# Kernel optimization log

Measured on AMD Instinct MI355X. Metric: run time of the kernel, lower is better.

## Reference

```python
import jax, jax.numpy as jnp
from jax import lax
import numpy as np

GAMMA = 0.5
LENS = 0.3
B_J0 = 0.1
# eval-mode BN with running_mean=0, running_var=1, weight=0.1, bias=0 -> pure scale
BN_SCALE = 0.1 / np.sqrt(1.0 + 1e-5)


def _gaussian(x, mu, sigma):
    return jnp.exp(-(x - mu) ** 2 / (2.0 * sigma ** 2)) / np.sqrt(2.0 * np.pi) / sigma


@jax.custom_vjp
def act_fun_adp(x):
    return (x > 0).astype(x.dtype)


def _act_fwd(x):
    return act_fun_adp(x), x


def _act_bwd(x, g):
    scale, hight = 6.0, 0.15
    temp = (_gaussian(x, 0.0, LENS) * (1.0 + hight)
            - _gaussian(x, LENS, scale * LENS) * hight
            - _gaussian(x, -LENS, scale * LENS) * hight)
    return (g * temp * GAMMA,)


act_fun_adp.defvjp(_act_fwd, _act_bwd)


def _lin(x, w, b):
    return x @ w.T + b


def _mem_update_adp(inp, mem, spk, tau_adp, tau_m, b):
    b = tau_adp * b + (1.0 - tau_adp) * spk
    B = B_J0 + 1.8 * b
    mem = mem + (-mem + inp) * tau_m
    spk = act_fun_adp(mem - B)
    mem = (1.0 - spk) * mem
    return mem, spk, b


def _snn(inputs, h, p):
    (w1x, b1x, w1r, b1r, w1m, b1m, w1a, b1a,
     w2x, b2x, w2r, b2r, w2m, b2m, w2a, b2a,
     w3x, b3x, w3m, b3m) = p

    def step(h, x):
        mem1, spk1, bb1, mem2, spk2, bb2, mem3 = h
        dense1 = BN_SCALE * _lin(x, w1x, b1x) + BN_SCALE * _lin(spk1, w1r, b1r)
        tauM1 = jax.nn.sigmoid(_lin(jnp.concatenate([dense1, mem1], -1), w1m, b1m))
        tauA1 = jax.nn.sigmoid(_lin(jnp.concatenate([dense1, bb1], -1), w1a, b1a))
        nmem1, nspk1, nbb1 = _mem_update_adp(dense1, mem1, spk1, tauA1, tauM1, bb1)
        # dropout in eval mode = identity; layer2_r uses PREVIOUS spk1 (h[1]) as in source
        dense2 = BN_SCALE * _lin(nspk1, w2x, b2x) + BN_SCALE * _lin(spk1, w2r, b2r)
        tauM2 = jax.nn.sigmoid(_lin(jnp.concatenate([dense2, mem2], -1), w2m, b2m))
        tauA2 = jax.nn.sigmoid(_lin(jnp.concatenate([dense2, bb2], -1), w2a, b2a))
        nmem2, nspk2, nbb2 = _mem_update_adp(dense2, mem2, spk2, tauA2, tauM2, bb2)
        dense3 = BN_SCALE * _lin(nspk2, w3x, b3x)
        tauM3 = jax.nn.sigmoid(_lin(jnp.concatenate([dense3, mem3], -1), w3m, b3m))
        nmem3 = (1.0 - tauM3) * mem3 + dense3 * tauM3
        out = jax.nn.log_softmax(nmem3, axis=1)
        return (nmem1, nspk1, nbb1, nmem2, nspk2, nbb2, nmem3), out

    xs = jnp.swapaxes(inputs, 0, 1)  # [T, B, Din]
    hT, outs = lax.scan(step, h, xs)
    return outs, hT  # outs: [T, B, O]


def setup_inputs() -> dict:
    key = jax.random.key(0)
    B, T, DIN, H, O = 128, 100, 700, 1024, 20
    ks = jax.random.split(key, 16)
    d = {
        'inputs': jax.random.normal(ks[0], (B, T, DIN), jnp.float32),
        'h0': jnp.zeros((B, H)), 'h1': jnp.zeros((B, H)), 'h2': jnp.zeros((B, H)),
        'h3': jnp.zeros((B, H)), 'h4': jnp.zeros((B, H)), 'h5': jnp.zeros((B, H)),
        'h6': jnp.zeros((B, O)),
        'w1x': jax.random.normal(ks[1], (H, DIN)) * 0.03,
        'b1x': jnp.zeros((H,)),
        'w1r': jax.random.normal(ks[2], (H, H)) * 0.03,
        'b1r': jnp.zeros((H,)),
        'w1m': jax.random.normal(ks[3], (H, 2 * H)) * 0.02,
        'b1m': jnp.zeros((H,)),
        'w1a': jax.random.normal(ks[4], (H, 2 * H)) * 0.02,
        'b1a': jnp.zeros((H,)),
        'w2x': jax.random.normal(ks[5], (H, H)) * 0.03,
        'b2x': jnp.zeros((H,)),
        'w2r': jax.random.normal(ks[6], (H, H)) * 0.03,
        'b2r': jnp.zeros((H,)),
        'w2m': jax.random.normal(ks[7], (H, 2 * H)) * 0.02,
        'b2m': jnp.zeros((H,)),
        'w2a': jax.random.normal(ks[8], (H, 2 * H)) * 0.02,
        'b2a': jnp.zeros((H,)),
        'w3x': jax.random.normal(ks[9], (O, H)) * 0.03,
        'b3x': jnp.zeros((O,)),
        'w3m': jax.random.normal(ks[10], (O, 2 * O)) * 0.02,
        'b3m': jnp.zeros((O,)),
    }
    return d


def reference(inputs, h0, h1, h2, h3, h4, h5, h6,
              w1x, b1x, w1r, b1r, w1m, b1m, w1a, b1a,
              w2x, b2x, w2r, b2r, w2m, b2m, w2a, b2a,
              w3x, b3x, w3m, b3m):
    h = (h0, h1, h2, h3, h4, h5, h6)
    p = (w1x, b1x, w1r, b1r, w1m, b1m, w1a, b1a,
         w2x, b2x, w2r, b2r, w2m, b2m, w2a, b2a,
         w3x, b3x, w3m, b3m)
    outs, hT = _snn(inputs, h, p)
    return (outs,) + hT
```

## Files before the change

### kernel.cpp

```cpp
#include <hip/hip_runtime.h>
#include <cmath>


namespace {

constexpr int BB = 128, TT = 100, DIN = 700, HH = 1024, OO = 20;
constexpr int BH = BB * HH;
constexpr int XP = 704;
constexpr float SBN = 0.09999950000374996f;

typedef __attribute__((ext_vector_type(8))) __bf16 bf16x8;
typedef __attribute__((ext_vector_type(4))) float f32x4;

__device__ __forceinline__ float sigm(float x) { return 1.f / (1.f + expf(-x)); }

__device__ __forceinline__ unsigned short f2bf(float x) {
  union { float f; unsigned u; } a; a.f = x;
  unsigned u = a.u; u += 0x7fffu + ((u >> 16) & 1u);
  return (unsigned short)(u >> 16);
}
__device__ __forceinline__ float bf2f(unsigned short h) {
  union { unsigned u; float f; } a; a.u = ((unsigned)h) << 16; return a.f;
}


struct MSeg {
  const unsigned short* Ah; const unsigned short* Al;
  const unsigned short* Wh; const unsigned short* Wl;
  float* P;
  int ldk, KS, nsplit, nblkn;
};
struct MArgs { MSeg s[6]; int bstart[7]; int nseg; };

__global__ __launch_bounds__(256)
void mfma_seg(MArgs ma) {
  int bid = blockIdx.x, si = 0;
  while (si + 1 < ma.nseg && bid >= ma.bstart[si + 1]) si++;
  MSeg sg = ma.s[si]; bid -= ma.bstart[si];
  const int nb = bid / sg.nsplit, sp = bid - nb * sg.nsplit;
  const int n0 = nb * 64;
  const int kbeg = sp * sg.KS, kend = kbeg + sg.KS;
  const int lane = threadIdx.x & 63, wave = threadIdx.x >> 6;
  const int wm = (wave >> 1) * 64, wn = (wave & 1) * 32;
  const int quad = lane >> 4, r16 = lane & 15;
  const int ldk = sg.ldk;
  const int nkb = ldk >> 5;
  const bool three = (sg.Al != nullptr);
  const unsigned short* ah = sg.Ah + (size_t)(wm + r16) * ldk + quad * 8;
  const unsigned short* al = three ? sg.Al + (size_t)(wm + r16) * ldk + quad * 8 : ah;
  const size_t tb = (size_t)((n0 + wn) >> 4) * nkb * 512 + (size_t)lane * 8;
  const unsigned short* wh = sg.Wh + tb;
  const unsigned short* wl = sg.Wl + tb;

  f32x4 acc[4][2];
#pragma unroll
  for (int i = 0; i < 4; i++)
#pragma unroll
    for (int j = 0; j < 2; j++) acc[i][j] = (f32x4){0.f, 0.f, 0.f, 0.f};

  auto loadf = [&](int k, bf16x8* Ab, bf16x8* ALb, bf16x8* Bb, bf16x8* BLb) {
    const int kb = k >> 5;
#pragma unroll
    for (int mt = 0; mt < 4; mt++)
      Ab[mt] = *(const bf16x8*)(ah + (size_t)mt * 16 * ldk + k);
#pragma unroll
    for (int nt = 0; nt < 2; nt++) {
      Bb[nt] = *(const bf16x8*)(wh + ((size_t)nt * nkb + kb) * 512);
      BLb[nt] = *(const bf16x8*)(wl + ((size_t)nt * nkb + kb) * 512);
    }
    if (three) {
#pragma unroll
      for (int mt = 0; mt < 4; mt++)
        ALb[mt] = *(const bf16x8*)(al + (size_t)mt * 16 * ldk + k);
    }
  };
  auto domfma = [&](bf16x8* Ab, bf16x8* ALb, bf16x8* Bb, bf16x8* BLb) {
#pragma unroll
    for (int mt = 0; mt < 4; mt++)
#pragma unroll
      for (int nt = 0; nt < 2; nt++) {
        acc[mt][nt] = __builtin_amdgcn_mfma_f32_16x16x32_bf16(Ab[mt], Bb[nt], acc[mt][nt], 0, 0, 0);
        acc[mt][nt] = __builtin_amdgcn_mfma_f32_16x16x32_bf16(Ab[mt], BLb[nt], acc[mt][nt], 0, 0, 0);
        if (three)
          acc[mt][nt] = __builtin_amdgcn_mfma_f32_16x16x32_bf16(ALb[mt], Bb[nt], acc[mt][nt], 0, 0, 0);
      }
  };

  bf16x8 A0[4], L0[4], B0[2], C0[2];
  bf16x8 A1[4], L1[4], B1[2], C1[2];
  int k = kbeg;
  loadf(k, A0, L0, B0, C0);
  while (true) {
    int k1 = k + 32;
    bool more1 = k1 < kend;
    if (more1) loadf(k1, A1, L1, B1, C1);
    domfma(A0, L0, B0, C0);
    if (!more1) break;
    int k2 = k1 + 32;
    bool more2 = k2 < kend;
    if (more2) loadf(k2, A0, L0, B0, C0);
    domfma(A1, L1, B1, C1);
    if (!more2) break;
    k = k2;
  }

  const int outl = n0 >> 10;
  const int col0 = (n0 & 1023) + wn;
  float* P = sg.P + (size_t)(outl * sg.nsplit + sp) * BH;
#pragma unroll
  for (int mt = 0; mt < 4; mt++)
#pragma unroll
    for (int nt = 0; nt < 2; nt++)
#pragma unroll
      for (int r = 0; r < 4; r++)
        P[(size_t)(wm + mt * 16 + quad * 4 + r) * 1024 + col0 + nt * 16 + r16] = acc[mt][nt][r];
}

struct CJob { const float* src; int ldsrc, rows, cols; unsigned short* dh; unsigned short* dl; int lddst; float scale; };
struct CArgs { CJob j[16]; int bstart[17]; int njob; };

__global__ __launch_bounds__(256)
void cvt_pack(CArgs ca) {
  int bid = blockIdx.x, ji = 0;
  while (ji + 1 < ca.njob && bid >= ca.bstart[ji + 1]) ji++;
  CJob j = ca.j[ji]; bid -= ca.bstart[ji];
  size_t total = (size_t)j.rows * j.lddst;
  size_t base = ((size_t)bid * 256 + threadIdx.x) * 4;
  const int nkb = j.lddst >> 5;
#pragma unroll
  for (int e = 0; e < 4; e++) {
    size_t i = base + e;
    if (i >= total) break;
    size_t tile = i >> 9;
    int within = (int)(i & 511);
    int lane = within >> 3, jj = within & 7;
    int r16 = lane & 15, quad = lane >> 4;
    int ntile = (int)(tile / nkb), kb = (int)(tile - (size_t)ntile * nkb);
    int r = ntile * 16 + r16;
    int c = kb * 32 + quad * 8 + jj;
    float v = (c < j.cols) ? j.scale * j.src[(size_t)r * j.ldsrc + c] : 0.f;
    unsigned short hh = f2bf(v);
    j.dh[i] = hh;
    j.dl[i] = f2bf(v - bf2f(hh));
  }
}

__global__ __launch_bounds__(256)
void init_state(const float* h0, const float* h1, const float* h2, const float* h3,
                const float* h4, const float* h5, const float* h6, const float* inputs,
                float* mem1, float* spk1, float* bb1, float* mem2, float* spk2, float* bb2,
                float* mem3, unsigned short* spk1bf,
                unsigned short* m1h, unsigned short* m1l, unsigned short* b1h, unsigned short* b1l,
                unsigned short* m2h, unsigned short* m2l, unsigned short* b2h, unsigned short* b2l,
                unsigned short* xh0, unsigned short* xl0) {
  int idx = blockIdx.x * 256 + threadIdx.x;
  if (idx < BH) {
    float v;
    v = h0[idx]; mem1[idx] = v; { unsigned short h = f2bf(v); m1h[idx] = h; m1l[idx] = f2bf(v - bf2f(h)); }
    v = h1[idx]; spk1[idx] = v; spk1bf[idx] = f2bf(v);
    v = h2[idx]; bb1[idx] = v;  { unsigned short h = f2bf(v); b1h[idx] = h; b1l[idx] = f2bf(v - bf2f(h)); }
    v = h3[idx]; mem2[idx] = v; { unsigned short h = f2bf(v); m2h[idx] = h; m2l[idx] = f2bf(v - bf2f(h)); }
    spk2[idx] = h4[idx];
    v = h5[idx]; bb2[idx] = v;  { unsigned short h = f2bf(v); b2h[idx] = h; b2l[idx] = f2bf(v - bf2f(h)); }
  }
  if (idx < BB * OO) mem3[idx] = h6[idx];
  if (idx < BB * XP) {
    int b = idx / XP, c = idx - b * XP;
    float v = (c < DIN) ? inputs[(size_t)b * TT * DIN + c] : 0.f;
    unsigned short hh = f2bf(v);
    xh0[idx] = hh; xl0[idx] = f2bf(v - bf2f(hh));
  }
}

__global__ __launch_bounds__(256)
void ew1m(const float* Pbuf, const float* b1x, const float* b1r,
          const float* cb1m, const float* cb1a,
          float* mem1, float* spk1, float* bb1, unsigned short* spk1bf,
          unsigned short* m1h, unsigned short* m1l, unsigned short* b1h_, unsigned short* b1l_) {
  int idx = blockIdx.x * 256 + threadIdx.x;
  int n = idx & (HH - 1);
  constexpr int D1S[6]  = {0, 1, 6, 7, 8, 9};
  constexpr int T1MS[10] = {2, 3, 10, 11, 12, 13, 30, 31, 32, 33};
  constexpr int T1AS[10] = {4, 5, 14, 15, 16, 17, 34, 35, 36, 37};
  float d1 = SBN * (b1x[n] + b1r[n]);
#pragma unroll
  for (int i = 0; i < 6; i++) d1 += Pbuf[(size_t)D1S[i] * BH + idx];
  float pm = cb1m[n];
#pragma unroll
  for (int i = 0; i < 10; i++) pm += Pbuf[(size_t)T1MS[i] * BH + idx];
  float pa = cb1a[n];
#pragma unroll
  for (int i = 0; i < 10; i++) pa += Pbuf[(size_t)T1AS[i] * BH + idx];
  float tM = sigm(pm), tA = sigm(pa);
  float spo = spk1[idx], bo = bb1[idx], mo = mem1[idx];
  float nb = tA * bo + (1.f - tA) * spo;
  float Bth = 0.1f + 1.8f * nb;
  float nm = mo + (d1 - mo) * tM;
  float sp = (nm - Bth) > 0.f ? 1.f : 0.f;
  nm = (1.f - sp) * nm;
  mem1[idx] = nm; spk1[idx] = sp; bb1[idx] = nb;
  spk1bf[idx] = f2bf(sp);
  { unsigned short h = f2bf(nm); m1h[idx] = h; m1l[idx] = f2bf(nm - bf2f(h)); }
  { unsigned short h = f2bf(nb); b1h_[idx] = h; b1l_[idx] = f2bf(nb - bf2f(h)); }
}

__global__ __launch_bounds__(1024)
void ew2l3m(const float* Pbuf, const float* b2x, const float* b2r,
            const float* cb2m, const float* cb2a,
            float* mem2, float* spk2, float* bb2, float* mem3,
            unsigned short* m2h, unsigned short* m2l, unsigned short* b2h_, unsigned short* b2l_,
            const float* w3x, const float* b3x, const float* w3m, const float* b3m,
            float* outs, const float* inputs, unsigned short* xh_next, unsigned short* xl_next,
            int t) {
  int b = blockIdx.x;
  int n = threadIdx.x;
  size_t idx = (size_t)b * HH + n;
  constexpr int D2S[8]  = {18, 19, 20, 21, 46, 47, 48, 49};
  constexpr int T2MS[12] = {22, 23, 24, 25, 38, 39, 40, 41, 50, 51, 52, 53};
  constexpr int T2AS[12] = {26, 27, 28, 29, 42, 43, 44, 45, 54, 55, 56, 57};
  float d2 = SBN * (b2x[n] + b2r[n]);
#pragma unroll
  for (int i = 0; i < 8; i++) d2 += Pbuf[(size_t)D2S[i] * BH + idx];
  float pm = cb2m[n];
#pragma unroll
  for (int i = 0; i < 12; i++) pm += Pbuf[(size_t)T2MS[i] * BH + idx];
  float pa = cb2a[n];
#pragma unroll
  for (int i = 0; i < 12; i++) pa += Pbuf[(size_t)T2AS[i] * BH + idx];
  float tM = sigm(pm), tA = sigm(pa);
  float spo = spk2[idx], bo = bb2[idx], mo = mem2[idx];
  float nb = tA * bo + (1.f - tA) * spo;
  float Bth = 0.1f + 1.8f * nb;
  float nm = mo + (d2 - mo) * tM;
  float sp = (nm - Bth) > 0.f ? 1.f : 0.f;
  nm = (1.f - sp) * nm;
  mem2[idx] = nm; spk2[idx] = sp; bb2[idx] = nb;
  { unsigned short h = f2bf(nm); m2h[idx] = h; m2l[idx] = f2bf(nm - bf2f(h)); }
  { unsigned short h = f2bf(nb); b2h_[idx] = h; b2l_[idx] = f2bf(nb - bf2f(h)); }

  if (t + 1 < TT && n < XP) {
    float v = (n < DIN) ? inputs[((size_t)b * TT + (t + 1)) * DIN + n] : 0.f;
    unsigned short hh = f2bf(v);
    xh_next[b * XP + n] = hh;
    xl_next[b * XP + n] = f2bf(v - bf2f(hh));
  }

  __shared__ float smsp[HH];
  __shared__ float d3s[OO];
  __shared__ float nm3s[OO];
  smsp[n] = sp;
  __syncthreads();

  int wv = n >> 6, ln = n & 63;
  for (int o = wv; o < OO; o += 16) {
    float s = 0.f;
    for (int j = ln; j < HH; j += 64) s += smsp[j] * w3x[(size_t)o * HH + j];
    for (int off = 32; off > 0; off >>= 1) s += __shfl_down(s, off, 64);
    if (ln == 0) d3s[o] = SBN * (s + b3x[o]);
  }
  __syncthreads();

  if (n < OO) {
    float acc = b3m[n];
#pragma unroll
    for (int k = 0; k < OO; k++) acc += d3s[k] * w3m[n * 40 + k];
#pragma unroll
    for (int k = 0; k < OO; k++) acc += mem3[b * OO + k] * w3m[n * 40 + 20 + k];
    float tau = sigm(acc);
    nm3s[n] = (1.f - tau) * mem3[b * OO + n] + d3s[n] * tau;
  }
  __syncthreads();

  if (n < OO) {
    float mx = -1e30f;
#pragma unroll
    for (int k = 0; k < OO; k++) mx = fmaxf(mx, nm3s[k]);
    float se = 0.f;
#pragma unroll
    for (int k = 0; k < OO; k++) se += expf(nm3s[k] - mx);
    float lse = mx + logf(se);
    outs[((size_t)t * BB + b) * OO + n] = nm3s[n] - lse;
    mem3[b * OO + n] = nm3s[n];
  }
}


struct Seg {
  const float* A; const float* W; float* P;
  int lda, ldw, ldp, K, KS, nsplit, mblks, nblks, nbound, xmap, xoff;
  float scale;
};
constexpr int MAXSEG = 13;
struct SegArgs { Seg s[MAXSEG]; int bstart[MAXSEG + 1]; int nseg; };

__global__ __launch_bounds__(256)
void seg_gemm(SegArgs sa) {
  int bid = blockIdx.x;
  int si = 0;
  while (si + 1 < sa.nseg && bid >= sa.bstart[si + 1]) si++;
  const Seg sg = sa.s[si];
  bid -= sa.bstart[si];
  const int per_m = sg.nblks * sg.nsplit;
  const int mb = bid / per_m;
  const int rr = bid - mb * per_m;
  const int nb = rr / sg.nsplit;
  const int sp = rr - nb * sg.nsplit;
  const int m0 = mb * 128, n0 = nb * 32;
  const int kbeg = sp * sg.KS;
  const int kend = min(sg.K, kbeg + sg.KS);

  __shared__ float As[32][132];
  __shared__ float Ws[32][36];

  const int t = threadIdx.x;
  const int cg = t & 7;
  const int rg = t >> 3;

  float acc[4][4];
#pragma unroll
  for (int i = 0; i < 4; i++)
#pragma unroll
    for (int j = 0; j < 4; j++) acc[i][j] = 0.f;

  for (int k0 = kbeg; k0 < kend; k0 += 32) {
#pragma unroll
    for (int i = 0; i < 4; i++) {
      int fl = t + i * 256;
      int row = fl >> 3, kq = fl & 7;
      int kg = k0 + kq * 4;
      float4 v = make_float4(0.f, 0.f, 0.f, 0.f);
      if (kg < kend) {
        const float* src = sg.xmap
            ? sg.A + ((size_t)(m0 + row) * TT + sg.xoff) * DIN + kg
            : sg.A + (size_t)(m0 + row) * sg.lda + kg;
        v = *(const float4*)src;
      }
      As[kq * 4 + 0][row] = v.x;
      As[kq * 4 + 1][row] = v.y;
      As[kq * 4 + 2][row] = v.z;
      As[kq * 4 + 3][row] = v.w;
    }
    {
      int n = t >> 3, kq = t & 7;
      int kg = k0 + kq * 4;
      float4 v = make_float4(0.f, 0.f, 0.f, 0.f);
      if (kg < kend && (n0 + n) < sg.nbound)
        v = *(const float4*)(sg.W + (size_t)(n0 + n) * sg.ldw + kg);
      Ws[kq * 4 + 0][n] = v.x;
      Ws[kq * 4 + 1][n] = v.y;
      Ws[kq * 4 + 2][n] = v.z;
      Ws[kq * 4 + 3][n] = v.w;
    }
    __syncthreads();
#pragma unroll
    for (int kk = 0; kk < 32; kk++) {
      float4 av = *(const float4*)&As[kk][rg * 4];
      float4 wv = *(const float4*)&Ws[kk][cg * 4];
      acc[0][0] += av.x * wv.x; acc[0][1] += av.x * wv.y; acc[0][2] += av.x * wv.z; acc[0][3] += av.x * wv.w;
      acc[1][0] += av.y * wv.x; acc[1][1] += av.y * wv.y; acc[1][2] += av.y * wv.z; acc[1][3] += av.y * wv.w;
      acc[2][0] += av.z * wv.x; acc[2][1] += av.z * wv.y; acc[2][2] += av.z * wv.z; acc[2][3] += av.z * wv.w;
      acc[3][0] += av.w * wv.x; acc[3][1] += av.w * wv.y; acc[3][2] += av.w * wv.z; acc[3][3] += av.w * wv.w;
    }
    __syncthreads();
  }
  float* P = sg.P + ((size_t)sp * sg.mblks * 128 + m0) * sg.ldp;
#pragma unroll
  for (int i = 0; i < 4; i++) {
    float4 v = make_float4(sg.scale * acc[i][0], sg.scale * acc[i][1],
                           sg.scale * acc[i][2], sg.scale * acc[i][3]);
    *(float4*)&P[(size_t)(rg * 4 + i) * sg.ldp + n0 + cg * 4] = v;
  }
}

struct TJob { const float* src; float* dst; int rows, cols, ntc; };
struct TArgs { TJob j[4]; int tstart[5]; };

__global__ __launch_bounds__(256)
void transpose4(TArgs ta) {
  int bid = blockIdx.x;
  int ji = 0;
  while (ji + 1 < 4 && bid >= ta.tstart[ji + 1]) ji++;
// ... 463 lines not shown
    ta.j[0] = TJob{w1r, w1rT, HH, HH, 32};
    ta.j[1] = TJob{w2r, w2rT, HH, HH, 32};
    ta.j[2] = TJob{w2x, w2xT, HH, HH, 32};
    ta.j[3] = TJob{w1x, w1xT, HH, DIN, 22};
    ta.tstart[0] = 0; ta.tstart[1] = 1024; ta.tstart[2] = 2048;
    ta.tstart[3] = 3072; ta.tstart[4] = 3072 + 32 * 22;
    transpose4<<<ta.tstart[4], 256, 0, stream>>>(ta);
  }
  bias_prep<<<1024, 256, 0, stream>>>(b1x, b1r, b2x, b2r, w1m, b1m, w1a, b1a,
                                      w2m, b2m, w2a, b2a, cb1m, cb1a, cb2m, cb2a);
  {
    SegArgs sa{};
    int nb = 0, c = 0;
    auto add = [&](const float* A, int lda, const float* W, int ldw, int nbound,
                   float* P, int ldp, int nblks) {
      sa.s[c] = Seg{A, W, P, lda, ldw, ldp, HH, HH, 1, 8, nblks, nbound, 0, 0, 1.0f};
      sa.bstart[c] = nb; nb += 8 * nblks; c++;
    };
    add(w1m, 2048, w1rT, 1024, 1024, G1mT, 1024, 32);
    add(w1a, 2048, w1rT, 1024, 1024, G1aT, 1024, 32);
    add(w1m, 2048, w1xT, 1024, DIN, H1MT, 704, 22);
    add(w1a, 2048, w1xT, 1024, DIN, H1AT, 704, 22);
    add(w2m, 2048, w2rT, 1024, 1024, G2rmT, 1024, 32);
    add(w2a, 2048, w2rT, 1024, 1024, G2raT, 1024, 32);
    add(w2m, 2048, w2xT, 1024, 1024, G2xmT, 1024, 32);
    add(w2a, 2048, w2xT, 1024, 1024, G2xaT, 1024, 32);
    sa.bstart[c] = nb; sa.nseg = c;
    seg_gemm<<<nb, 256, 0, stream>>>(sa);
  }

  for (int t = 0; t < TT; ++t) {
    {
      SegArgs sa{};
      int nb = 0, c = 0;
      auto add = [&](const float* A, int lda, int xmap, const float* W, int ldw,
                     int K, int KS, int slot, float scale) {
        sa.s[c] = Seg{A, W, Pbuf + (size_t)slot * BH, lda, ldw, 1024, K, KS, 2, 1, 32,
                      1024, xmap, t, scale};
        sa.bstart[c] = nb; nb += 64; c++;
      };
      add(inputs, 0, 1, w1x, DIN, DIN, 352, 0, SBN);
      add(spk1, 1024, 0, w1r, 1024, 1024, 512, 2, SBN);
      add(inputs, 0, 1, H1MT, 704, DIN, 352, 4, SBN);
      add(spk1, 1024, 0, G1mT, 1024, 1024, 512, 6, SBN);
      add(mem1, 1024, 0, w1m + 1024, 2048, 1024, 512, 8, 1.0f);
      add(inputs, 0, 1, H1AT, 704, DIN, 352, 10, SBN);
      add(spk1, 1024, 0, G1aT, 1024, 1024, 512, 12, SBN);
      add(bb1, 1024, 0, w1a + 1024, 2048, 1024, 512, 14, 1.0f);
      add(spk1, 1024, 0, w2r, 1024, 1024, 512, 16, SBN);
      add(spk1, 1024, 0, G2rmT, 1024, 1024, 512, 18, SBN);
      add(mem2, 1024, 0, w2m + 1024, 2048, 1024, 512, 20, 1.0f);
      add(spk1, 1024, 0, G2raT, 1024, 1024, 512, 22, SBN);
      add(bb2, 1024, 0, w2a + 1024, 2048, 1024, 512, 24, 1.0f);
      sa.bstart[c] = nb; sa.nseg = c;
      seg_gemm<<<nb, 256, 0, stream>>>(sa);
    }
    ew1<<<BH / 256, 256, 0, stream>>>(Pbuf, b1x, b1r, cb1m, cb1a, mem1, spk1, bb1);
    {
      SegArgs sa{};
      int nb = 0, c = 0;
      auto add = [&](const float* W, int slot) {
        sa.s[c] = Seg{spk1, W, Pbuf + (size_t)slot * BH, 1024, 1024, 1024, 1024, 512,
                      2, 1, 32, 1024, 0, 0, SBN};
        sa.bstart[c] = nb; nb += 64; c++;
      };
      add(w2x, 26);
      add(G2xmT, 28);
      add(G2xaT, 30);
      sa.bstart[c] = nb; sa.nseg = c;
      seg_gemm<<<nb, 256, 0, stream>>>(sa);
    }
    ew2_layer3<<<BB, 1024, 0, stream>>>(Pbuf, b2x, b2r, cb2m, cb2a, mem2, spk2, bb2,
                                        mem3, w3x, b3x, w3m, b3m, (float*)d_out, t);
  }

  float* out = (float*)d_out;
  size_t o = (size_t)TT * BB * OO;
  hipMemcpyAsync(out + o, mem1, (size_t)BH * 4, hipMemcpyDeviceToDevice, stream); o += BH;
  hipMemcpyAsync(out + o, spk1, (size_t)BH * 4, hipMemcpyDeviceToDevice, stream); o += BH;
  hipMemcpyAsync(out + o, bb1,  (size_t)BH * 4, hipMemcpyDeviceToDevice, stream); o += BH;
  hipMemcpyAsync(out + o, mem2, (size_t)BH * 4, hipMemcpyDeviceToDevice, stream); o += BH;
  hipMemcpyAsync(out + o, spk2, (size_t)BH * 4, hipMemcpyDeviceToDevice, stream); o += BH;
  hipMemcpyAsync(out + o, bb2,  (size_t)BH * 4, hipMemcpyDeviceToDevice, stream); o += BH;
  hipMemcpyAsync(out + o, mem3, (size_t)BB * OO * 4, hipMemcpyDeviceToDevice, stream);
}

}

extern "C" void kernel_launch(void* const* d_in, const int* in_sizes, int n_in,
                              void* d_out, int out_size, void* d_ws, size_t ws_size,
                              hipStream_t stream) {
  const float* inputs = (const float*)d_in[0];
  const float* h0 = (const float*)d_in[1]; const float* h1 = (const float*)d_in[2];
  const float* h2 = (const float*)d_in[3]; const float* h3 = (const float*)d_in[4];
  const float* h4 = (const float*)d_in[5]; const float* h5 = (const float*)d_in[6];
  const float* h6 = (const float*)d_in[7];
  const float* w1x = (const float*)d_in[8];  const float* b1x = (const float*)d_in[9];
  const float* w1r = (const float*)d_in[10]; const float* b1r = (const float*)d_in[11];
  const float* w1m = (const float*)d_in[12]; const float* b1m = (const float*)d_in[13];
  const float* w1a = (const float*)d_in[14]; const float* b1a = (const float*)d_in[15];
  const float* w2x = (const float*)d_in[16]; const float* b2x = (const float*)d_in[17];
  const float* w2r = (const float*)d_in[18]; const float* b2r = (const float*)d_in[19];
  const float* w2m = (const float*)d_in[20]; const float* b2m = (const float*)d_in[21];
  const float* w2a = (const float*)d_in[22]; const float* b2a = (const float*)d_in[23];
  const float* w3x = (const float*)d_in[24]; const float* b3x = (const float*)d_in[25];
  const float* w3m = (const float*)d_in[26]; const float* b3m = (const float*)d_in[27];

  char* base = (char*)d_ws;
  size_t cur = 0;
  auto alloc = [&](size_t bytes) -> char* {
    char* p = base + cur;
    cur += (bytes + 255) & ~(size_t)255;
    return p;
  };
  float* mem1 = (float*)alloc((size_t)BH * 4);
  float* spk1 = (float*)alloc((size_t)BH * 4);
  float* bb1  = (float*)alloc((size_t)BH * 4);
  float* mem2 = (float*)alloc((size_t)BH * 4);
  float* spk2 = (float*)alloc((size_t)BH * 4);
  float* bb2  = (float*)alloc((size_t)BH * 4);
  float* mem3 = (float*)alloc((size_t)BB * OO * 4);
  float* cb1m = (float*)alloc(HH * 4);
  float* cb1a = (float*)alloc(HH * 4);
  float* cb2m = (float*)alloc(HH * 4);
  float* cb2a = (float*)alloc(HH * 4);
  unsigned short* spk1bf = (unsigned short*)alloc((size_t)BH * 2);
  unsigned short* m1h = (unsigned short*)alloc((size_t)BH * 2);
  unsigned short* m1l = (unsigned short*)alloc((size_t)BH * 2);
  unsigned short* b1h = (unsigned short*)alloc((size_t)BH * 2);
  unsigned short* b1l = (unsigned short*)alloc((size_t)BH * 2);
  unsigned short* m2h = (unsigned short*)alloc((size_t)BH * 2);
  unsigned short* m2l = (unsigned short*)alloc((size_t)BH * 2);
  unsigned short* b2h = (unsigned short*)alloc((size_t)BH * 2);
  unsigned short* b2l = (unsigned short*)alloc((size_t)BH * 2);
  unsigned short* xh[2]; unsigned short* xl[2];
  xh[0] = (unsigned short*)alloc((size_t)BB * XP * 2);
  xl[0] = (unsigned short*)alloc((size_t)BB * XP * 2);
  xh[1] = (unsigned short*)alloc((size_t)BB * XP * 2);
  xl[1] = (unsigned short*)alloc((size_t)BB * XP * 2);
  unsigned short* XWh  = (unsigned short*)alloc((size_t)3 * HH * XP * 2);
  unsigned short* XWl  = (unsigned short*)alloc((size_t)3 * HH * XP * 2);
  unsigned short* WSPKh = (unsigned short*)alloc((size_t)6 * HH * HH * 2);
  unsigned short* WSPKl = (unsigned short*)alloc((size_t)6 * HH * HH * 2);
  unsigned short* WM1h = (unsigned short*)alloc((size_t)HH * HH * 2);
  unsigned short* WM1l = (unsigned short*)alloc((size_t)HH * HH * 2);
  unsigned short* WB1h = (unsigned short*)alloc((size_t)HH * HH * 2);
  unsigned short* WB1l = (unsigned short*)alloc((size_t)HH * HH * 2);
  unsigned short* WM2h = (unsigned short*)alloc((size_t)HH * HH * 2);
  unsigned short* WM2l = (unsigned short*)alloc((size_t)HH * HH * 2);
  unsigned short* WB2h = (unsigned short*)alloc((size_t)HH * HH * 2);
  unsigned short* WB2l = (unsigned short*)alloc((size_t)HH * HH * 2);
  unsigned short* WSBh = (unsigned short*)alloc((size_t)3 * HH * HH * 2);
  unsigned short* WSBl = (unsigned short*)alloc((size_t)3 * HH * HH * 2);
  size_t scratch_fl = (size_t)3 * HH * HH + (size_t)DIN * HH
                    + (size_t)6 * HH * HH + (size_t)2 * HH * XP;
  size_t pbuf_fl = (size_t)58 * BH;
  size_t shared_fl = scratch_fl > pbuf_fl ? scratch_fl : pbuf_fl;
  char* shared = alloc(shared_fl * 4);

  if (ws_size < cur) {
    launch_tier2(d_in, d_out, d_ws, ws_size, stream);
    return;
  }

  float* w1rT = (float*)shared;
  float* w2rT = w1rT + (size_t)HH * HH;
  float* w2xT = w2rT + (size_t)HH * HH;
  float* w1xT = w2xT + (size_t)HH * HH;
  float* G1m  = w1xT + (size_t)DIN * HH;
  float* G1a  = G1m + (size_t)HH * HH;
  float* G2rm = G1a + (size_t)HH * HH;
  float* G2ra = G2rm + (size_t)HH * HH;
  float* G2xm = G2ra + (size_t)HH * HH;
  float* G2xa = G2xm + (size_t)HH * HH;
  float* H1M  = G2xa + (size_t)HH * HH;
  float* H1A  = H1M + (size_t)HH * XP;
  float* Pbuf = (float*)shared;

  init_state<<<BH / 256, 256, 0, stream>>>(h0, h1, h2, h3, h4, h5, h6, inputs,
      mem1, spk1, bb1, mem2, spk2, bb2, mem3, spk1bf,
      m1h, m1l, b1h, b1l, m2h, m2l, b2h, b2l, xh[0], xl[0]);

  {
    TArgs ta{};
    ta.j[0] = TJob{w1r, w1rT, HH, HH, 32};
    ta.j[1] = TJob{w2r, w2rT, HH, HH, 32};
    ta.j[2] = TJob{w2x, w2xT, HH, HH, 32};
    ta.j[3] = TJob{w1x, w1xT, HH, DIN, 22};
    ta.tstart[0] = 0; ta.tstart[1] = 1024; ta.tstart[2] = 2048;
    ta.tstart[3] = 3072; ta.tstart[4] = 3072 + 32 * 22;
    transpose4<<<ta.tstart[4], 256, 0, stream>>>(ta);
  }

  bias_prep<<<1024, 256, 0, stream>>>(b1x, b1r, b2x, b2r, w1m, b1m, w1a, b1a,
                                      w2m, b2m, w2a, b2a, cb1m, cb1a, cb2m, cb2a);

  {
    SegArgs sa{};
    int nb = 0, c = 0;
    auto add = [&](const float* A, const float* W, int nbound, float* P, int ldp, int nblks) {
      sa.s[c] = Seg{A, W, P, 2048, 1024, ldp, HH, HH, 1, 8, nblks, nbound, 0, 0, SBN};
      sa.bstart[c] = nb; nb += 8 * nblks; c++;
    };
    add(w1m, w1rT, 1024, G1m, 1024, 32);
    add(w1a, w1rT, 1024, G1a, 1024, 32);
    add(w2m, w2rT, 1024, G2rm, 1024, 32);
    add(w2a, w2rT, 1024, G2ra, 1024, 32);
    add(w2m, w2xT, 1024, G2xm, 1024, 32);
    add(w2a, w2xT, 1024, G2xa, 1024, 32);
    add(w1m, w1xT, DIN, H1M, XP, 22);
    add(w1a, w1xT, DIN, H1A, XP, 22);
    sa.bstart[c] = nb; sa.nseg = c;
    seg_gemm<<<nb, 256, 0, stream>>>(sa);
  }

  {
    CArgs ca{};
    int nb = 0, c = 0;
    auto add = [&](const float* src, int ldsrc, int rows, int cols,
                   unsigned short* dh, unsigned short* dl, int lddst, float scale) {
      ca.j[c] = CJob{src, ldsrc, rows, cols, dh, dl, lddst, scale};
      ca.bstart[c] = nb;
      nb += (int)(((size_t)rows * lddst + 1023) / 1024);
      c++;
    };
    add(w1x, DIN, HH, DIN, XWh, XWl, XP, SBN);
    add(H1M, XP, HH, XP, XWh + (size_t)HH * XP, XWl + (size_t)HH * XP, XP, 1.f);
    add(H1A, XP, HH, XP, XWh + (size_t)2 * HH * XP, XWl + (size_t)2 * HH * XP, XP, 1.f);
    add(w1r, HH, HH, HH, WSPKh, WSPKl, HH, SBN);
    add(G1m, HH, HH, HH, WSPKh + (size_t)HH * HH, WSPKl + (size_t)HH * HH, HH, 1.f);
    add(G1a, HH, HH, HH, WSPKh + (size_t)2 * HH * HH, WSPKl + (size_t)2 * HH * HH, HH, 1.f);
    add(w2r, HH, HH, HH, WSPKh + (size_t)3 * HH * HH, WSPKl + (size_t)3 * HH * HH, HH, SBN);
    add(G2rm, HH, HH, HH, WSPKh + (size_t)4 * HH * HH, WSPKl + (size_t)4 * HH * HH, HH, 1.f);
    add(G2ra, HH, HH, HH, WSPKh + (size_t)5 * HH * HH, WSPKl + (size_t)5 * HH * HH, HH, 1.f);
    add(w1m + 1024, 2048, HH, HH, WM1h, WM1l, HH, 1.f);
    add(w1a + 1024, 2048, HH, HH, WB1h, WB1l, HH, 1.f);
    add(w2m + 1024, 2048, HH, HH, WM2h, WM2l, HH, 1.f);
    add(w2a + 1024, 2048, HH, HH, WB2h, WB2l, HH, 1.f);
    add(w2x, HH, HH, HH, WSBh, WSBl, HH, SBN);
    add(G2xm, HH, HH, HH, WSBh + (size_t)HH * HH, WSBl + (size_t)HH * HH, HH, 1.f);
    add(G2xa, HH, HH, HH, WSBh + (size_t)2 * HH * HH, WSBl + (size_t)2 * HH * HH, HH, 1.f);
    ca.bstart[c] = nb; ca.njob = c;
    cvt_pack<<<nb, 256, 0, stream>>>(ca);
  }

  for (int t = 0; t < TT; ++t) {
    {
      MArgs ma{};
      int nb = 0, c = 0;
      auto add = [&](const unsigned short* Ah, const unsigned short* Al,
                     const unsigned short* Wh, const unsigned short* Wl,
                     int ldk, int KS, int nsplit, int nblkn, int baseslot) {
        ma.s[c] = MSeg{Ah, Al, Wh, Wl, Pbuf + (size_t)baseslot * BH, ldk, KS, nsplit, nblkn};
        ma.bstart[c] = nb; nb += nblkn * nsplit; c++;
      };
      add(xh[t & 1], xl[t & 1], XWh, XWl, XP, 352, 2, 48, 0);
      add(spk1bf, nullptr, WSPKh, WSPKl, HH, 256, 4, 96, 6);
      add(m1h, m1l, WM1h, WM1l, HH, 256, 4, 16, 30);
      add(b1h, b1l, WB1h, WB1l, HH, 256, 4, 16, 34);
      add(m2h, m2l, WM2h, WM2l, HH, 256, 4, 16, 38);
      add(b2h, b2l, WB2h, WB2l, HH, 256, 4, 16, 42);
      ma.bstart[c] = nb; ma.nseg = c;
      mfma_seg<<<nb, 256, 0, stream>>>(ma);
    }
    ew1m<<<BH / 256, 256, 0, stream>>>(Pbuf, b1x, b1r, cb1m, cb1a,
                                       mem1, spk1, bb1, spk1bf, m1h, m1l, b1h, b1l);
    {
      MArgs ma{};
      ma.s[0] = MSeg{spk1bf, nullptr, WSBh, WSBl, Pbuf + (size_t)46 * BH, HH, 256, 4, 48};
      ma.bstart[0] = 0; ma.bstart[1] = 192; ma.nseg = 1;
      mfma_seg<<<192, 256, 0, stream>>>(ma);
    }
    ew2l3m<<<BB, 1024, 0, stream>>>(Pbuf, b2x, b2r, cb2m, cb2a,
                                    mem2, spk2, bb2, mem3, m2h, m2l, b2h, b2l,
                                    w3x, b3x, w3m, b3m, (float*)d_out,
                                    inputs, xh[(t + 1) & 1], xl[(t + 1) & 1], t);
  }

  float* out = (float*)d_out;
  size_t o = (size_t)TT * BB * OO;
  hipMemcpyAsync(out + o, mem1, (size_t)BH * 4, hipMemcpyDeviceToDevice, stream); o += BH;
  hipMemcpyAsync(out + o, spk1, (size_t)BH * 4, hipMemcpyDeviceToDevice, stream); o += BH;
  hipMemcpyAsync(out + o, bb1,  (size_t)BH * 4, hipMemcpyDeviceToDevice, stream); o += BH;
  hipMemcpyAsync(out + o, mem2, (size_t)BH * 4, hipMemcpyDeviceToDevice, stream); o += BH;
  hipMemcpyAsync(out + o, spk2, (size_t)BH * 4, hipMemcpyDeviceToDevice, stream); o += BH;
  hipMemcpyAsync(out + o, bb2,  (size_t)BH * 4, hipMemcpyDeviceToDevice, stream); o += BH;
  hipMemcpyAsync(out + o, mem3, (size_t)BB * OO * 4, hipMemcpyDeviceToDevice, stream);
}
```

Baseline: 6.367 ms.

## Move weight-fold precompute to split-bf16 MFMA and halve recurrent GEMM k-splits

```diff
diff --git a/kernel.cpp b/kernel.cpp
--- a/kernel.cpp
+++ b/kernel.cpp
@@ -28,17 +28,22 @@
   const unsigned short* Ah; const unsigned short* Al;
   const unsigned short* Wh; const unsigned short* Wl;
   float* P;
-  int ldk, KS, nsplit, nblkn;
+  int ldk, KS, nsplit, nblkn, mbs, ldp;
+  size_t planesz;
 };
-struct MArgs { MSeg s[6]; int bstart[7]; int nseg; };
+struct MArgs { MSeg s[8]; int bstart[9]; int nseg; };
 
 __global__ __launch_bounds__(256)
 void mfma_seg(MArgs ma) {
   int bid = blockIdx.x, si = 0;
   while (si + 1 < ma.nseg && bid >= ma.bstart[si + 1]) si++;
   MSeg sg = ma.s[si]; bid -= ma.bstart[si];
-  const int nb = bid / sg.nsplit, sp = bid - nb * sg.nsplit;
+  const int per_m = sg.nblkn * sg.nsplit;
+  const int mb = bid / per_m;
+  const int rr = bid - mb * per_m;
+  const int nb = rr / sg.nsplit, sp = rr - nb * sg.nsplit;
   const int n0 = nb * 64;
+  const int m0 = mb * 128;
   const int kbeg = sp * sg.KS, kend = kbeg + sg.KS;
   const int lane = threadIdx.x & 63, wave = threadIdx.x >> 6;
   const int wm = (wave >> 1) * 64, wn = (wave & 1) * 32;
@@ -46,8 +51,8 @@
   const int ldk = sg.ldk;
   const int nkb = ldk >> 5;
   const bool three = (sg.Al != nullptr);
-  const unsigned short* ah = sg.Ah + (size_t)(wm + r16) * ldk + quad * 8;
-  const unsigned short* al = three ? sg.Al + (size_t)(wm + r16) * ldk + quad * 8 : ah;
+  const unsigned short* ah = sg.Ah + (size_t)(m0 + wm + r16) * ldk + quad * 8;
+  const unsigned short* al = three ? sg.Al + (size_t)(m0 + wm + r16) * ldk + quad * 8 : ah;
   const size_t tb = (size_t)((n0 + wn) >> 4) * nkb * 512 + (size_t)lane * 8;
   const unsigned short* wh = sg.Wh + tb;
   const unsigned short* wl = sg.Wl + tb;
@@ -106,17 +111,17 @@
 
   const int outl = n0 >> 10;
   const int col0 = (n0 & 1023) + wn;
-  float* P = sg.P + (size_t)(outl * sg.nsplit + sp) * BH;
+  float* P = sg.P + (size_t)(outl * sg.nsplit + sp) * sg.planesz;
 #pragma unroll
   for (int mt = 0; mt < 4; mt++)
 #pragma unroll
     for (int nt = 0; nt < 2; nt++)
 #pragma unroll
       for (int r = 0; r < 4; r++)
-        P[(size_t)(wm + mt * 16 + quad * 4 + r) * 1024 + col0 + nt * 16 + r16] = acc[mt][nt][r];
-}
-
-struct CJob { const float* src; int ldsrc, rows, cols; unsigned short* dh; unsigned short* dl; int lddst; float scale; };
+        P[(size_t)(m0 + wm + mt * 16 + quad * 4 + r) * sg.ldp + col0 + nt * 16 + r16] = acc[mt][nt][r];
+}
+
+struct CJob { const float* src; int ldsrc, rows, cols, rrows, mode; unsigned short* dh; unsigned short* dl; int lddst; float scale; };
 struct CArgs { CJob j[16]; int bstart[17]; int njob; };
 
 __global__ __launch_bounds__(256)
@@ -131,14 +136,22 @@
   for (int e = 0; e < 4; e++) {
     size_t i = base + e;
     if (i >= total) break;
-    size_t tile = i >> 9;
-    int within = (int)(i & 511);
-    int lane = within >> 3, jj = within & 7;
-    int r16 = lane & 15, quad = lane >> 4;
-    int ntile = (int)(tile / nkb), kb = (int)(tile - (size_t)ntile * nkb);
-    int r = ntile * 16 + r16;
-    int c = kb * 32 + quad * 8 + jj;
-    float v = (c < j.cols) ? j.scale * j.src[(size_t)r * j.ldsrc + c] : 0.f;
+    int r, c;
+    if (j.mode == 2) {
+      r = (int)(i / j.lddst); c = (int)(i - (size_t)r * j.lddst);
+    } else {
+      size_t tile = i >> 9;
+      int within = (int)(i & 511);
+      int lane = within >> 3, jj = within & 7;
+      int r16 = lane & 15, quad = lane >> 4;
+      int ntile = (int)(tile / nkb), kb = (int)(tile - (size_t)ntile * nkb);
+      r = ntile * 16 + r16;
+      c = kb * 32 + quad * 8 + jj;
+    }
+    float v = 0.f;
+    if (c < j.cols && r < j.rrows)
+      v = j.scale * (j.mode == 1 ? j.src[(size_t)c * j.ldsrc + r]
+                                 : j.src[(size_t)r * j.ldsrc + c]);
     unsigned short hh = f2bf(v);
     j.dh[i] = hh;
     j.dl[i] = f2bf(v - bf2f(hh));
@@ -179,18 +192,18 @@
           unsigned short* m1h, unsigned short* m1l, unsigned short* b1h_, unsigned short* b1l_) {
   int idx = blockIdx.x * 256 + threadIdx.x;
   int n = idx & (HH - 1);
-  constexpr int D1S[6]  = {0, 1, 6, 7, 8, 9};
-  constexpr int T1MS[10] = {2, 3, 10, 11, 12, 13, 30, 31, 32, 33};
-  constexpr int T1AS[10] = {4, 5, 14, 15, 16, 17, 34, 35, 36, 37};
+  constexpr int D1S[4]  = {0, 1, 6, 7};
+  constexpr int T1MS[6] = {2, 3, 8, 9, 18, 19};
+  constexpr int T1AS[6] = {4, 5, 10, 11, 20, 21};
   float d1 = SBN * (b1x[n] + b1r[n]);
 #pragma unroll
-  for (int i = 0; i < 6; i++) d1 += Pbuf[(size_t)D1S[i] * BH + idx];
+  for (int i = 0; i < 4; i++) d1 += Pbuf[(size_t)D1S[i] * BH + idx];
   float pm = cb1m[n];
 #pragma unroll
-  for (int i = 0; i < 10; i++) pm += Pbuf[(size_t)T1MS[i] * BH + idx];
+  for (int i = 0; i < 6; i++) pm += Pbuf[(size_t)T1MS[i] * BH + idx];
   float pa = cb1a[n];
 #pragma unroll
-  for (int i = 0; i < 10; i++) pa += Pbuf[(size_t)T1AS[i] * BH + idx];
+  for (int i = 0; i < 6; i++) pa += Pbuf[(size_t)T1AS[i] * BH + idx];
   float tM = sigm(pm), tA = sigm(pa);
   float spo = spk1[idx], bo = bb1[idx], mo = mem1[idx];
   float nb = tA * bo + (1.f - tA) * spo;
@@ -215,18 +228,18 @@
   int b = blockIdx.x;
   int n = threadIdx.x;
   size_t idx = (size_t)b * HH + n;
-  constexpr int D2S[8]  = {18, 19, 20, 21, 46, 47, 48, 49};
-  constexpr int T2MS[12] = {22, 23, 24, 25, 38, 39, 40, 41, 50, 51, 52, 53};
-  constexpr int T2AS[12] = {26, 27, 28, 29, 42, 43, 44, 45, 54, 55, 56, 57};
+  constexpr int D2S[6]  = {12, 13, 26, 27, 28, 29};
+  constexpr int T2MS[8] = {14, 15, 22, 23, 30, 31, 32, 33};
+  constexpr int T2AS[8] = {16, 17, 24, 25, 34, 35, 36, 37};
   float d2 = SBN * (b2x[n] + b2r[n]);
 #pragma unroll
-  for (int i = 0; i < 8; i++) d2 += Pbuf[(size_t)D2S[i] * BH + idx];
+  for (int i = 0; i < 6; i++) d2 += Pbuf[(size_t)D2S[i] * BH + idx];
   float pm = cb2m[n];
 #pragma unroll
-  for (int i = 0; i < 12; i++) pm += Pbuf[(size_t)T2MS[i] * BH + idx];
+  for (int i = 0; i < 8; i++) pm += Pbuf[(size_t)T2MS[i] * BH + idx];
   float pa = cb2a[n];
 #pragma unroll
-  for (int i = 0; i < 12; i++) pa += Pbuf[(size_t)T2AS[i] * BH + idx];
+  for (int i = 0; i < 8; i++) pa += Pbuf[(size_t)T2AS[i] * BH + idx];
   float tM = sigm(pm), tA = sigm(pa);
   float spo = spk2[idx], bo = bb2[idx], mo = mem2[idx];
   float nb = tA * bo + (1.f - tA) * spo;
@@ -996,9 +1009,8 @@
   unsigned short* WB2l = (unsigned short*)alloc((size_t)HH * HH * 2);
   unsigned short* WSBh = (unsigned short*)alloc((size_t)3 * HH * HH * 2);
   unsigned short* WSBl = (unsigned short*)alloc((size_t)3 * HH * HH * 2);
-  size_t scratch_fl = (size_t)3 * HH * HH + (size_t)DIN * HH
-                    + (size_t)6 * HH * HH + (size_t)2 * HH * XP;
-  size_t pbuf_fl = (size_t)58 * BH;
+  size_t scratch_fl = (size_t)6 * HH * HH + (size_t)2 * HH * XP;
+  size_t pbuf_fl = (size_t)38 * BH;
   size_t shared_fl = scratch_fl > pbuf_fl ? scratch_fl : pbuf_fl;
   char* shared = alloc(shared_fl * 4);
 
@@ -1007,11 +1019,7 @@
     return;
   }
 
-  float* w1rT = (float*)shared;
-  float* w2rT = w1rT + (size_t)HH * HH;
-  float* w2xT = w2rT + (size_t)HH * HH;
-  float* w1xT = w2xT + (size_t)HH * HH;
-  float* G1m  = w1xT + (size_t)DIN * HH;
+  float* G1m  = (float*)shared;
   float* G1a  = G1m + (size_t)HH * HH;
   float* G2rm = G1a + (size_t)HH * HH;
   float* G2ra = G2rm + (size_t)HH * HH;
@@ -1021,41 +1029,71 @@
   float* H1A  = H1M + (size_t)HH * XP;
   float* Pbuf = (float*)shared;
 
+  unsigned short* opW1rTh = WSPKh;
+  unsigned short* opW1rTl = WSPKh + (size_t)1 * HH * HH;
+  unsigned short* opW2rTh = WSPKh + (size_t)2 * HH * HH;
+  unsigned short* opW2rTl = WSPKh + (size_t)3 * HH * HH;
+  unsigned short* opW2xTh = WSPKh + (size_t)4 * HH * HH;
+  unsigned short* opW2xTl = WSPKh + (size_t)5 * HH * HH;
+  unsigned short* opW1xTh = WSPKl;
+  unsigned short* opW1xTl = WSPKl + (size_t)XP * HH;
+  unsigned short* opW1mh  = WSPKl + (size_t)2 * XP * HH;
+  unsigned short* opW1ml  = opW1mh + (size_t)HH * HH;
+  unsigned short* opW1ah  = opW1ml + (size_t)HH * HH;
+  unsigned short* opW1al  = opW1ah + (size_t)HH * HH;
+  unsigned short* opW2mh  = WM1h;
+  unsigned short* opW2ml  = WM1l;
+  unsigned short* opW2ah  = WB1h;
+  unsigned short* opW2al  = WB1l;
+
   init_state<<<BH / 256, 256, 0, stream>>>(h0, h1, h2, h3, h4, h5, h6, inputs,
       mem1, spk1, bb1, mem2, spk2, bb2, mem3, spk1bf,
       m1h, m1l, b1h, b1l, m2h, m2l, b2h, b2l, xh[0], xl[0]);
 
-  {
-    TArgs ta{};
-    ta.j[0] = TJob{w1r, w1rT, HH, HH, 32};
-    ta.j[1] = TJob{w2r, w2rT, HH, HH, 32};
-    ta.j[2] = TJob{w2x, w2xT, HH, HH, 32};
-    ta.j[3] = TJob{w1x, w1xT, HH, DIN, 22};
-    ta.tstart[0] = 0; ta.tstart[1] = 1024; ta.tstart[2] = 2048;
-    ta.tstart[3] = 3072; ta.tstart[4] = 3072 + 32 * 22;
-    transpose4<<<ta.tstart[4], 256, 0, stream>>>(ta);
-  }
-
   bias_prep<<<1024, 256, 0, stream>>>(b1x, b1r, b2x, b2r, w1m, b1m, w1a, b1a,
                                       w2m, b2m, w2a, b2a, cb1m, cb1a, cb2m, cb2a);
 
   {
-    SegArgs sa{};
+    CArgs ca{};
     int nb = 0, c = 0;
-    auto add = [&](const float* A, const float* W, int nbound, float* P, int ldp, int nblks) {
-      sa.s[c] = Seg{A, W, P, 2048, 1024, ldp, HH, HH, 1, 8, nblks, nbound, 0, 0, SBN};
-      sa.bstart[c] = nb; nb += 8 * nblks; c++;
+    auto add = [&](const float* src, int ldsrc, int rows, int cols, int rrows, int mode,
+                   unsigned short* dh, unsigned short* dl, int lddst, float scale) {
+      ca.j[c] = CJob{src, ldsrc, rows, cols, rrows, mode, dh, dl, lddst, scale};
+      ca.bstart[c] = nb;
+      nb += (int)(((size_t)rows * lddst + 1023) / 1024);
+      c++;
     };
-    add(w1m, w1rT, 1024, G1m, 1024, 32);
-    add(w1a, w1rT, 1024, G1a, 1024, 32);
-    add(w2m, w2rT, 1024, G2rm, 1024, 32);
-    add(w2a, w2rT, 1024, G2ra, 1024, 32);
-    add(w2m, w2xT, 1024, G2xm, 1024, 32);
-    add(w2a, w2xT, 1024, G2xa, 1024, 32);
-    add(w1m, w1xT, DIN, H1M, XP, 22);
-    add(w1a, w1xT, DIN, H1A, XP, 22);
-    sa.bstart[c] = nb; sa.nseg = c;
-    seg_gemm<<<nb, 256, 0, stream>>>(sa);
+    add(w1r, HH, HH, HH, HH, 1, opW1rTh, opW1rTl, HH, SBN);
+    add(w2r, HH, HH, HH, HH, 1, opW2rTh, opW2rTl, HH, SBN);
+    add(w2x, HH, HH, HH, HH, 1, opW2xTh, opW2xTl, HH, SBN);
+    add(w1x, DIN, XP, HH, DIN, 1, opW1xTh, opW1xTl, HH, SBN);
+    add(w1m, 2048, HH, HH, HH, 2, opW1mh, opW1ml, HH, 1.f);
+    add(w1a, 2048, HH, HH, HH, 2, opW1ah, opW1al, HH, 1.f);
+    add(w2m, 2048, HH, HH, HH, 2, opW2mh, opW2ml, HH, 1.f);
+    add(w2a, 2048, HH, HH, HH, 2, opW2ah, opW2al, HH, 1.f);
+    ca.bstart[c] = nb; ca.njob = c;
+    cvt_pack<<<nb, 256, 0, stream>>>(ca);
+  }
+
+  {
+    MArgs ma{};
+    int nb = 0, c = 0;
+    auto add = [&](const unsigned short* Ah, const unsigned short* Al,
+                   const unsigned short* Wh, const unsigned short* Wl,
+                   float* P, int nblkn, int ldp) {
+      ma.s[c] = MSeg{Ah, Al, Wh, Wl, P, HH, HH, 1, nblkn, 8, ldp, (size_t)HH * HH};
+      ma.bstart[c] = nb; nb += 8 * nblkn; c++;
+    };
+    add(opW1mh, opW1ml, opW1rTh, opW1rTl, G1m, 16, HH);
+    add(opW1ah, opW1al, opW1rTh, opW1rTl, G1a, 16, HH);
+    add(opW2mh, opW2ml, opW2rTh, opW2rTl, G2rm, 16, HH);
+    add(opW2ah, opW2al, opW2rTh, opW2rTl, G2ra, 16, HH);
+    add(opW2mh, opW2ml, opW2xTh, opW2xTl, G2xm, 16, HH);
+    add(opW2ah, opW2al, opW2xTh, opW2xTl, G2xa, 16, HH);
+    add(opW1mh, opW1ml, opW1xTh, opW1xTl, H1M, 11, XP);
+    add(opW1ah, opW1al, opW1xTh, opW1xTl, H1A, 11, XP);
+    ma.bstart[c] = nb; ma.nseg = c;
+    mfma_seg<<<nb, 256, 0, stream>>>(ma);
   }
 
   {
@@ -1063,7 +1101,7 @@
     int nb = 0, c = 0;
     auto add = [&](const float* src, int ldsrc, int rows, int cols,
                    unsigned short* dh, unsigned short* dl, int lddst, float scale) {
-      ca.j[c] = CJob{src, ldsrc, rows, cols, dh, dl, lddst, scale};
+      ca.j[c] = CJob{src, ldsrc, rows, cols, rows, 0, dh, dl, lddst, scale};
       ca.bstart[c] = nb;
       nb += (int)(((size_t)rows * lddst + 1023) / 1024);
       c++;
@@ -1095,15 +1133,16 @@
       auto add = [&](const unsigned short* Ah, const unsigned short* Al,
                      const unsigned short* Wh, const unsigned short* Wl,
                      int ldk, int KS, int nsplit, int nblkn, int baseslot) {
-        ma.s[c] = MSeg{Ah, Al, Wh, Wl, Pbuf + (size_t)baseslot * BH, ldk, KS, nsplit, nblkn};
+        ma.s[c] = MSeg{Ah, Al, Wh, Wl, Pbuf + (size_t)baseslot * BH, ldk, KS, nsplit,
+                       nblkn, 1, 1024, (size_t)BH};
         ma.bstart[c] = nb; nb += nblkn * nsplit; c++;
       };
       add(xh[t & 1], xl[t & 1], XWh, XWl, XP, 352, 2, 48, 0);
-      add(spk1bf, nullptr, WSPKh, WSPKl, HH, 256, 4, 96, 6);
-      add(m1h, m1l, WM1h, WM1l, HH, 256, 4, 16, 30);
-      add(b1h, b1l, WB1h, WB1l, HH, 256, 4, 16, 34);
-      add(m2h, m2l, WM2h, WM2l, HH, 256, 4, 16, 38);
-      add(b2h, b2l, WB2h, WB2l, HH, 256, 4, 16, 42);
+      add(spk1bf, nullptr, WSPKh, WSPKl, HH, 512, 2, 96, 6);
+      add(m1h, m1l, WM1h, WM1l, HH, 512, 2, 16, 18);
+      add(b1h, b1l, WB1h, WB1l, HH, 512, 2, 16, 20);
+      add(m2h, m2l, WM2h, WM2l, HH, 512, 2, 16, 22);
+      add(b2h, b2l, WB2h, WB2l, HH, 512, 2, 16, 24);
       ma.bstart[c] = nb; ma.nseg = c;
       mfma_seg<<<nb, 256, 0, stream>>>(ma);
     }
@@ -1111,7 +1150,8 @@
                                        mem1, spk1, bb1, spk1bf, m1h, m1l, b1h, b1l);
     {
       MArgs ma{};
-      ma.s[0] = MSeg{spk1bf, nullptr, WSBh, WSBl, Pbuf + (size_t)46 * BH, HH, 256, 4, 48};
+      ma.s[0] = MSeg{spk1bf, nullptr, WSBh, WSBl, Pbuf + (size_t)26 * BH, HH, 256, 4,
+                     48, 1, 1024, (size_t)BH};
       ma.bstart[0] = 0; ma.bstart[1] = 192; ma.nseg = 1;
       mfma_seg<<<192, 256, 0, stream>>>(ma);
     }
```

New measurement: 6.370 ms. About the same (+0.1%).
